# Optimization experiments

Hardware: AMD Instinct MI355X
Metric: run time of the kernel (lower is better)

The kernel has to match this reference:

```python
import jax, jax.numpy as jnp
import numpy as np

DELTA = 1e-08
P = 3
Q = 3
M = 128   # ctrl pts in u
N = 128   # ctrl pts in v
OUT_U = 1024
OUT_V = 1024
DIM = 3
BATCH = 4


def gen_knot_vector(p, n_ctrl):
    # clamped uniform knot vector, length n_ctrl + p + 1 (NURBSDiff convention)
    return np.concatenate([np.zeros(p), np.linspace(0.0, 1.0, n_ctrl - p + 1), np.ones(p)]).astype(np.float64)


def find_span(n_ctrl, p, u, U):
    # NURBS book A2.1
    n = n_ctrl - 1
    if u >= U[n + 1]:
        return n
    if u <= U[p]:
        return p
    low, high = p, n + 1
    mid = (low + high) // 2
    while u < U[mid] or u >= U[mid + 1]:
        if u < U[mid]:
            high = mid
        else:
            low = mid
        mid = (low + high) // 2
    return mid


def basis_funs(i, u, p, U):
    # NURBS book A2.2 (Cox-de Boor)
    Nf = np.zeros(p + 1)
    Nf[0] = 1.0
    left = np.zeros(p + 1)
    right = np.zeros(p + 1)
    for j in range(1, p + 1):
        left[j] = u - U[i + 1 - j]
        right[j] = U[i + j] - u
        saved = 0.0
        for r in range(j):
            temp = Nf[r] / (right[r + 1] + left[j - r])
            Nf[r] = saved + right[r + 1] * temp
            saved = left[j - r] * temp
        Nf[j] = saved
    return Nf


def precompute(p, n_ctrl, out_dim):
    U = gen_knot_vector(p, n_ctrl)
    params = np.linspace(0.0 + DELTA, 1.0 - DELTA, out_dim)
    spans = np.empty(out_dim, dtype=np.int32)
    basis = np.empty((out_dim, p + 1), dtype=np.float32)
    for k, u in enumerate(params):
        s = find_span(n_ctrl, p, u, U)
        spans[k] = s
        basis[k] = basis_funs(s, u, p, U)
    return spans, basis


def setup_inputs() -> dict:
    key = jax.random.key(0)
    uspan, Nu = precompute(P, M, OUT_U)
    vspan, Nv = precompute(Q, N, OUT_V)
    ctrl_pts = jax.random.normal(key, (BATCH, M, N, DIM + 1), dtype=jnp.float32)
    # keep homogeneous weight channel positive & away from 0 to avoid divide blowup
    ctrl_pts = ctrl_pts.at[..., DIM].set(1.0 + 0.1 * jax.nn.sigmoid(ctrl_pts[..., DIM]))
    return {
        "ctrl_pts": ctrl_pts,
        "Nu": jnp.asarray(Nu),            # [OUT_U, P+1]
        "Nv": jnp.asarray(Nv),            # [OUT_V, Q+1]
        "uspan": jnp.asarray(uspan),      # [OUT_U] int32
        "vspan": jnp.asarray(vspan),      # [OUT_V] int32
    }


def reference(ctrl_pts, Nu, Nv, uspan, vspan):
    p = Nu.shape[1] - 1
    q = Nv.shape[1] - 1
    # local control-point index windows
    uidx = uspan[:, None] - p + jnp.arange(p + 1)  # [U, p+1]
    vidx = vspan[:, None] - q + jnp.arange(q + 1)  # [V, q+1]
    # gather along u and contract with u-basis: [B,U,p+1,n,D] -> [B,U,n,D]
    gu = ctrl_pts[:, uidx]                         # [B, U, p+1, n, D]
    tu = jnp.einsum('ul,bulnd->bund', Nu, gu)      # [B, U, n, D]
    # gather along v and contract with v-basis: [B,U,V,q+1,D] -> [B,U,V,D]
    gv = tu[:, :, vidx]                            # [B, U, V, q+1, D]
    sw = jnp.einsum('vr,buvrd->buvd', Nv, gv)      # [B, U, V, D] homogeneous
    return sw[..., :DIM] / sw[..., DIM:DIM + 1]
```

## Files before the change

kernel.cpp:

```cpp
#include <hip/hip_runtime.h>


#define OUT_U 1024
#define OUT_V 1024
#define MCTRL 128
#define NCTRL 128

typedef float vfloat3 __attribute__((ext_vector_type(3), aligned(4)));

__device__ __forceinline__ void fma4(float4& acc, float w, const float4& a) {
    acc.x = fmaf(w, a.x, acc.x);
    acc.y = fmaf(w, a.y, acc.y);
    acc.z = fmaf(w, a.z, acc.z);
    acc.w = fmaf(w, a.w, acc.w);
}

__global__ __launch_bounds__(256) void surf_eval_kernel(
    const float4* __restrict__ ctrl,
    const float4* __restrict__ Nu,
    const float4* __restrict__ Nv,
    const int*    __restrict__ uspan,
    const int*    __restrict__ vspan,
    float*        __restrict__ out)
{
    __shared__ float4 tu[NCTRL];

    const int bu  = blockIdx.x;
    const int b   = bu >> 10;
    const int u   = bu & 1023;
    const int tid = threadIdx.x;

    const int   us = uspan[u];
    const float4 nu = Nu[u];

    if (tid < NCTRL) {
        const float4* row = ctrl + ((size_t)(b * MCTRL + (us - 3)) * NCTRL) + tid;
        float4 a0 = row[0];
        float4 a1 = row[NCTRL];
        float4 a2 = row[2 * NCTRL];
        float4 a3 = row[3 * NCTRL];
        float4 acc;
        acc.x = nu.x * a0.x; acc.y = nu.x * a0.y;
        acc.z = nu.x * a0.z; acc.w = nu.x * a0.w;
        fma4(acc, nu.y, a1);
        fma4(acc, nu.z, a2);
        fma4(acc, nu.w, a3);
        tu[tid] = acc;
    }
    __syncthreads();

    const size_t outrow = (size_t)bu * OUT_V;
#pragma unroll
    for (int k = 0; k < 4; ++k) {
        const int v  = tid + k * 256;
        const int vs = vspan[v];
        const float4 nv = Nv[v];

        const float4 t0 = tu[vs - 3];
        const float4 t1 = tu[vs - 2];
        const float4 t2 = tu[vs - 1];
        const float4 t3 = tu[vs];

        float4 acc;
        acc.x = nv.x * t0.x; acc.y = nv.x * t0.y;
        acc.z = nv.x * t0.z; acc.w = nv.x * t0.w;
        fma4(acc, nv.y, t1);
        fma4(acc, nv.z, t2);
        fma4(acc, nv.w, t3);

        const float inv = __builtin_amdgcn_rcpf(acc.w);
        vfloat3 res;
        res.x = acc.x * inv;
        res.y = acc.y * inv;
        res.z = acc.z * inv;
        *(vfloat3*)(out + (outrow + (size_t)v) * 3) = res;
    }
}

extern "C" void kernel_launch(void* const* d_in, const int* in_sizes, int n_in,
                              void* d_out, int out_size, void* d_ws, size_t ws_size,
                              hipStream_t stream) {
    const float4* ctrl  = (const float4*)d_in[0];
    const float4* Nu    = (const float4*)d_in[1];
    const float4* Nv    = (const float4*)d_in[2];
    const int*    uspan = (const int*)d_in[3];
    const int*    vspan = (const int*)d_in[4];
    float*        out   = (float*)d_out;

    const int nblocks = 4 * OUT_U;
    surf_eval_kernel<<<nblocks, 256, 0, stream>>>(ctrl, Nu, Nv, uspan, vspan, out);
}
```

Baseline: 15.65 us.

## Process two output rows per block with prefetched ctrl loads and nontemporal stores

Each block now handles two u-rows instead of one. The v-span and Nv values are loaded into registers once and reused for both rows, and the control-point loads for the next row are issued before the current row's v-pass. Output stores become nontemporal. The aim is to amortise per-block setup and index loads, overlap global loads with compute, and avoid cache pollution from the write-heavy output, at the cost of fewer blocks and more registers.

```diff
diff --git a/kernel.cpp b/kernel.cpp
--- a/kernel.cpp
+++ b/kernel.cpp
@@ -5,6 +5,7 @@
 #define OUT_V 1024
 #define MCTRL 128
 #define NCTRL 128
+#define ROWS 2
 
 typedef float vfloat3 __attribute__((ext_vector_type(3), aligned(4)));
 
@@ -23,57 +24,86 @@
     const int*    __restrict__ vspan,
     float*        __restrict__ out)
 {
-    __shared__ float4 tu[NCTRL];
+    __shared__ float4 tu[ROWS][NCTRL];
 
-    const int bu  = blockIdx.x;
-    const int b   = bu >> 10;
-    const int u   = bu & 1023;
     const int tid = threadIdx.x;
+    const int bu0 = blockIdx.x * ROWS;
 
-    const int   us = uspan[u];
-    const float4 nu = Nu[u];
-
-    if (tid < NCTRL) {
-        const float4* row = ctrl + ((size_t)(b * MCTRL + (us - 3)) * NCTRL) + tid;
-        float4 a0 = row[0];
-        float4 a1 = row[NCTRL];
-        float4 a2 = row[2 * NCTRL];
-        float4 a3 = row[3 * NCTRL];
-        float4 acc;
-        acc.x = nu.x * a0.x; acc.y = nu.x * a0.y;
-        acc.z = nu.x * a0.z; acc.w = nu.x * a0.w;
-        fma4(acc, nu.y, a1);
-        fma4(acc, nu.z, a2);
-        fma4(acc, nu.w, a3);
-        tu[tid] = acc;
-    }
-    __syncthreads();
-
-    const size_t outrow = (size_t)bu * OUT_V;
+    int    vs[4];
+    float4 nv[4];
 #pragma unroll
     for (int k = 0; k < 4; ++k) {
-        const int v  = tid + k * 256;
-        const int vs = vspan[v];
-        const float4 nv = Nv[v];
+        const int v = tid + k * 256;
+        vs[k] = vspan[v];
+        nv[k] = Nv[v];
+    }
 
-        const float4 t0 = tu[vs - 3];
-        const float4 t1 = tu[vs - 2];
-        const float4 t2 = tu[vs - 1];
-        const float4 t3 = tu[vs];
+    float4 a0, a1, a2, a3, nu;
+    if (tid < NCTRL) {
+        const int bu = bu0;
+        const int b  = bu >> 10;
+        const int u  = bu & 1023;
+        const int us = uspan[u];
+        nu = Nu[u];
+        const float4* row = ctrl + ((size_t)(b * MCTRL + (us - 3)) * NCTRL) + tid;
+        a0 = row[0];
+        a1 = row[NCTRL];
+        a2 = row[2 * NCTRL];
+        a3 = row[3 * NCTRL];
+    }
 
-        float4 acc;
-        acc.x = nv.x * t0.x; acc.y = nv.x * t0.y;
-        acc.z = nv.x * t0.z; acc.w = nv.x * t0.w;
-        fma4(acc, nv.y, t1);
-        fma4(acc, nv.z, t2);
-        fma4(acc, nv.w, t3);
+#pragma unroll
+    for (int r = 0; r < ROWS; ++r) {
+        const int bu = bu0 + r;
 
-        const float inv = __builtin_amdgcn_rcpf(acc.w);
-        vfloat3 res;
-        res.x = acc.x * inv;
-        res.y = acc.y * inv;
-        res.z = acc.z * inv;
-        *(vfloat3*)(out + (outrow + (size_t)v) * 3) = res;
+        if (tid < NCTRL) {
+            float4 acc;
+            acc.x = nu.x * a0.x; acc.y = nu.x * a0.y;
+            acc.z = nu.x * a0.z; acc.w = nu.x * a0.w;
+            fma4(acc, nu.y, a1);
+            fma4(acc, nu.z, a2);
+            fma4(acc, nu.w, a3);
+            tu[r][tid] = acc;
+
+            if (r + 1 < ROWS) {
+                const int bun = bu0 + r + 1;
+                const int bn  = bun >> 10;
+                const int un  = bun & 1023;
+                const int usn = uspan[un];
+                nu = Nu[un];
+                const float4* rown = ctrl + ((size_t)(bn * MCTRL + (usn - 3)) * NCTRL) + tid;
+                a0 = rown[0];
+                a1 = rown[NCTRL];
+                a2 = rown[2 * NCTRL];
+                a3 = rown[3 * NCTRL];
+            }
+        }
+        __syncthreads();
+
+        const size_t outrow = (size_t)bu * OUT_V;
+#pragma unroll
+        for (int k = 0; k < 4; ++k) {
+            const int v = tid + k * 256;
+
+            const float4 t0 = tu[r][vs[k] - 3];
+            const float4 t1 = tu[r][vs[k] - 2];
+            const float4 t2 = tu[r][vs[k] - 1];
+            const float4 t3 = tu[r][vs[k]];
+
+            float4 acc;
+            acc.x = nv[k].x * t0.x; acc.y = nv[k].x * t0.y;
+            acc.z = nv[k].x * t0.z; acc.w = nv[k].x * t0.w;
+            fma4(acc, nv[k].y, t1);
+            fma4(acc, nv[k].z, t2);
+            fma4(acc, nv[k].w, t3);
+
+            const float inv = __builtin_amdgcn_rcpf(acc.w);
+            vfloat3 res;
+            res.x = acc.x * inv;
+            res.y = acc.y * inv;
+            res.z = acc.z * inv;
+            __builtin_nontemporal_store(res, (vfloat3*)(out + (outrow + (size_t)v) * 3));
+        }
     }
 }
 
@@ -87,6 +117,6 @@
     const int*    vspan = (const int*)d_in[4];
     float*        out   = (float*)d_out;
 
-    const int nblocks = 4 * OUT_U;
+    const int nblocks = (4 * OUT_U) / ROWS;
     surf_eval_kernel<<<nblocks, 256, 0, stream>>>(ctrl, Nu, Nv, uspan, vspan, out);
 }
```

After: 15.75 us. Within noise of the previous version (+0.7%).

## Map batch to wavefronts and split v across blocks, drop block sync

Applied to the files above, without the earlier changes.

Each 256-thread block now handles one u row for all four batches, one wavefront per batch, and covers half of the v range. Each wavefront computes its own u-contracted row in its own shared-memory slice, so the block-wide barrier is removed and all threads take part in the first stage. Output stores are marked nontemporal. This halves the block count and shares the u-basis and span loads across batches. Each wavefront now recomputes its full 128-wide row for only half of the v outputs, which doubles that stage's work in total.

```diff
diff --git a/kernel.cpp b/kernel.cpp
--- a/kernel.cpp
+++ b/kernel.cpp
@@ -6,87 +6,76 @@
 #define MCTRL 128
 #define NCTRL 128
 
+typedef float f4 __attribute__((ext_vector_type(4)));
 typedef float vfloat3 __attribute__((ext_vector_type(3), aligned(4)));
 
-__device__ __forceinline__ void fma4(float4& acc, float w, const float4& a) {
-    acc.x = fmaf(w, a.x, acc.x);
-    acc.y = fmaf(w, a.y, acc.y);
-    acc.z = fmaf(w, a.z, acc.z);
-    acc.w = fmaf(w, a.w, acc.w);
-}
+__global__ __launch_bounds__(256) void surf_eval_kernel(
+    const f4*  __restrict__ ctrl,
+    const f4*  __restrict__ Nu,
+    const f4*  __restrict__ Nv,
+    const int* __restrict__ uspan,
+    const int* __restrict__ vspan,
+    float*     __restrict__ out)
+{
+    __shared__ f4 tu[4][NCTRL];
 
-__global__ __launch_bounds__(256) void surf_eval_kernel(
-    const float4* __restrict__ ctrl,
-    const float4* __restrict__ Nu,
-    const float4* __restrict__ Nv,
-    const int*    __restrict__ uspan,
-    const int*    __restrict__ vspan,
-    float*        __restrict__ out)
-{
-    __shared__ float4 tu[NCTRL];
+    const int tid  = threadIdx.x;
+    const int w    = tid >> 6;
+    const int lane = tid & 63;
+    const int u    = blockIdx.x >> 1;
+    const int half = blockIdx.x & 1;
 
-    const int bu  = blockIdx.x;
-    const int b   = bu >> 10;
-    const int u   = bu & 1023;
-    const int tid = threadIdx.x;
+    const int us = uspan[u];
+    const f4  nu = Nu[u];
 
-    const int   us = uspan[u];
-    const float4 nu = Nu[u];
+    const f4* win = ctrl + ((size_t)(w * MCTRL + (us - 3)) * NCTRL);
+#pragma unroll
+    for (int h = 0; h < 2; ++h) {
+        const int j = lane + h * 64;
+        f4 acc = nu.x * win[j];
+        acc += nu.y * win[NCTRL + j];
+        acc += nu.z * win[2 * NCTRL + j];
+        acc += nu.w * win[3 * NCTRL + j];
+        tu[w][j] = acc;
+    }
 
-    if (tid < NCTRL) {
-        const float4* row = ctrl + ((size_t)(b * MCTRL + (us - 3)) * NCTRL) + tid;
-        float4 a0 = row[0];
-        float4 a1 = row[NCTRL];
-        float4 a2 = row[2 * NCTRL];
-        float4 a3 = row[3 * NCTRL];
-        float4 acc;
-        acc.x = nu.x * a0.x; acc.y = nu.x * a0.y;
-        acc.z = nu.x * a0.z; acc.w = nu.x * a0.w;
-        fma4(acc, nu.y, a1);
-        fma4(acc, nu.z, a2);
-        fma4(acc, nu.w, a3);
-        tu[tid] = acc;
-    }
-    __syncthreads();
+    const size_t outrow = ((size_t)w * OUT_U + (size_t)u) * OUT_V;
+    const int    vbase  = (half << 9) + lane;
+#pragma unroll 4
+    for (int k = 0; k < 8; ++k) {
+        const int v  = vbase + (k << 6);
+        const int vs = vspan[v];
+        const f4  nv = Nv[v];
 
-    const size_t outrow = (size_t)bu * OUT_V;
-#pragma unroll
-    for (int k = 0; k < 4; ++k) {
-        const int v  = tid + k * 256;
-        const int vs = vspan[v];
-        const float4 nv = Nv[v];
+        const f4 t0 = tu[w][vs - 3];
+        const f4 t1 = tu[w][vs - 2];
+        const f4 t2 = tu[w][vs - 1];
+        const f4 t3 = tu[w][vs];
 
-        const float4 t0 = tu[vs - 3];
-        const float4 t1 = tu[vs - 2];
-        const float4 t2 = tu[vs - 1];
-        const float4 t3 = tu[vs];
-
-        float4 acc;
-        acc.x = nv.x * t0.x; acc.y = nv.x * t0.y;
-        acc.z = nv.x * t0.z; acc.w = nv.x * t0.w;
-        fma4(acc, nv.y, t1);
-        fma4(acc, nv.z, t2);
-        fma4(acc, nv.w, t3);
+        f4 acc = nv.x * t0;
+        acc += nv.y * t1;
+        acc += nv.z * t2;
+        acc += nv.w * t3;
 
         const float inv = __builtin_amdgcn_rcpf(acc.w);
         vfloat3 res;
         res.x = acc.x * inv;
         res.y = acc.y * inv;
         res.z = acc.z * inv;
-        *(vfloat3*)(out + (outrow + (size_t)v) * 3) = res;
+        __builtin_nontemporal_store(res, (vfloat3*)(out + (outrow + (size_t)v) * 3));
     }
 }
 
 extern "C" void kernel_launch(void* const* d_in, const int* in_sizes, int n_in,
                               void* d_out, int out_size, void* d_ws, size_t ws_size,
                               hipStream_t stream) {
-    const float4* ctrl  = (const float4*)d_in[0];
-    const float4* Nu    = (const float4*)d_in[1];
-    const float4* Nv    = (const float4*)d_in[2];
-    const int*    uspan = (const int*)d_in[3];
-    const int*    vspan = (const int*)d_in[4];
-    float*        out   = (float*)d_out;
+    const f4*  ctrl  = (const f4*)d_in[0];
+    const f4*  Nu    = (const f4*)d_in[1];
+    const f4*  Nv    = (const f4*)d_in[2];
+    const int* uspan = (const int*)d_in[3];
+    const int* vspan = (const int*)d_in[4];
+    float*     out   = (float*)d_out;
 
-    const int nblocks = 4 * OUT_U;
+    const int nblocks = OUT_U * 2;
     surf_eval_kernel<<<nblocks, 256, 0, stream>>>(ctrl, Nu, Nv, uspan, vspan, out);
 }
```

Result: slower. 15.98 us (+2.1%).
